# Performance work log

Hardware: AMD Instinct MI355X
Metric: run time of the kernel (lower is better)

Reference implementation:

```python
import jax, jax.numpy as jnp
import numpy as np

HEIGHT = 8
WIDTH = 8
C = 3
FEAT = HEIGHT * WIDTH * C  # 192
ENC = 16


def setup_inputs() -> dict:
    key = jax.random.key(0)
    k1, k2, k3, k4, k5 = jax.random.split(key, 5)
    B, H, W = 128, 256, 256
    x = jax.random.normal(k1, (B, C, H, W), dtype=jnp.float32)
    # torch Linear init ~ U(-1/sqrt(fan_in), 1/sqrt(fan_in))
    s1 = 1.0 / np.sqrt(FEAT)
    s2 = 1.0 / np.sqrt(ENC)
    W_enc = jax.random.uniform(k2, (ENC, FEAT), jnp.float32, -s1, s1)
    b_enc = jax.random.uniform(k3, (ENC,), jnp.float32, -s1, s1)
    W_dec = jax.random.uniform(k4, (FEAT, ENC), jnp.float32, -s2, s2)
    b_dec = jax.random.uniform(k5, (FEAT,), jnp.float32, -s2, s2)
    return {"x": x, "W_enc": W_enc, "b_enc": b_enc, "W_dec": W_dec, "b_dec": b_dec}


def reference(x, W_enc, b_enc, W_dec, b_dec):
    B, Cc, H, W = x.shape
    nh, nw = H // HEIGHT, W // WIDTH
    # Extract non-overlapping patches, flattened in (C, h, w) order to match
    # x[:, :, i:i+h, j:j+w].reshape(B, -1) in the original.
    xp = x.reshape(B, Cc, nh, HEIGHT, nw, WIDTH)
    xp = xp.transpose(0, 2, 4, 1, 3, 5).reshape(B, nh, nw, FEAT)  # [B,nh,nw,FEAT]
    h = jax.nn.relu(jnp.einsum('bijf,ef->bije', xp, W_enc) + b_enc)
    out = jax.nn.relu(jnp.einsum('bije,fe->bijf', h, W_dec) + b_dec)
    attention = jax.nn.softmax(out, axis=-1)
    out = attention * out
    # Scatter patches back into image layout.
    y = out.reshape(B, nh, nw, Cc, HEIGHT, WIDTH).transpose(0, 3, 1, 4, 2, 5)
    y = y.reshape(B, Cc, H, W)
    return y
```

## Files before the change

kernel.cpp:

```cpp
#include <hip/hip_runtime.h>


constexpr int NPATCH = 128 * 32 * 32;
constexpr float L2E  = 1.4426950408889634f;

__device__ __forceinline__ float rdlane(float v, int l) {
  return __uint_as_float(__builtin_amdgcn_readlane(__float_as_uint(v), l));
}

__global__ __launch_bounds__(512, 4) void spatial_attn(
    const float* __restrict__ x,
    const float* __restrict__ Wenc,
    const float* __restrict__ benc,
    const float* __restrict__ Wdec,
    const float* __restrict__ bdec,
    float* __restrict__ y)
{
  __shared__ float  encl[16 * 512];
  __shared__ float2 hl2[8 * 64];
  __shared__ float  sls[512];

  const int tid  = threadIdx.x;
  const int lane = tid & 63;
  const int wv   = __builtin_amdgcn_readfirstlane(tid >> 6);
  const int p    = blockIdx.x * 64 + lane;
  const int b    = p >> 10;
  const int ii   = (p >> 5) & 31;
  const int jj   = p & 31;
  const size_t base = (size_t)b * 196608 + (size_t)ii * 2048 + (size_t)jj * 8;

  float we[16];
  const int col = (lane < 24) ? lane : 0;
  #pragma unroll
  for (int e = 0; e < 16; ++e) we[e] = Wenc[e * 192 + wv * 24 + col];

  float2 xv2[12];
  #pragma unroll
  for (int t = 0; t < 3; ++t) {
    const int cr = 3 * wv + t;
    const float* src = x + base + (cr >> 3) * 65536 + (cr & 7) * 256;
    const float4 v0 = *(const float4*)(src);
    const float4 v1 = *(const float4*)(src + 4);
    xv2[t*4+0] = make_float2(v0.x, v0.y);
    xv2[t*4+1] = make_float2(v0.z, v0.w);
    xv2[t*4+2] = make_float2(v1.x, v1.y);
    xv2[t*4+3] = make_float2(v1.z, v1.w);
  }

  #pragma unroll
  for (int e = 0; e < 16; ++e) {
    float2 a2 = make_float2(0.0f, 0.0f);
    #pragma unroll
    for (int k = 0; k < 12; ++k) {
      a2.x = fmaf(rdlane(we[e], 2 * k),     xv2[k].x, a2.x);
      a2.y = fmaf(rdlane(we[e], 2 * k + 1), xv2[k].y, a2.y);
    }
    encl[e * 512 + tid] = a2.x + a2.y;
  }
  __syncthreads();

  {
    const int e0 = 2 * wv;
    const float* c0 = encl + e0 * 512 + lane;
    const float* c1 = c0 + 512;
    float a0 = c0[0], a1 = c1[0];
    #pragma unroll
    for (int w8 = 1; w8 < 8; ++w8) { a0 += c0[w8 * 64]; a1 += c1[w8 * 64]; }
    hl2[wv * 64 + lane] = make_float2(fmaxf(a0 + benc[e0],     0.0f),
                                      fmaxf(a1 + benc[e0 + 1], 0.0f));
  }
  __syncthreads();

  float2 h2[8];
  #pragma unroll
  for (int k = 0; k < 8; ++k) h2[k] = hl2[k * 64 + lane];

  float o[24];
  float s = 0.0f;
  #pragma unroll
  for (int q = 0; q < 24; ++q) {
    const int f = wv * 24 + q;
    const float2* w2 = (const float2*)(Wdec + f * 16);
    float2 a2 = make_float2(bdec[f], 0.0f);
    #pragma unroll
    for (int k = 0; k < 8; ++k) {
      a2.x = fmaf(w2[k].x, h2[k].x, a2.x);
      a2.y = fmaf(w2[k].y, h2[k].y, a2.y);
    }
    float v = fmaxf(a2.x + a2.y, 0.0f);
    o[q] = v;
    s += __builtin_amdgcn_exp2f(v * L2E);
  }

  sls[tid] = s;
  __syncthreads();
  float st = sls[lane];
  #pragma unroll
  for (int w8 = 1; w8 < 8; ++w8) st += sls[w8 * 64 + lane];
  const float inv = __builtin_amdgcn_rcpf(st);

  #pragma unroll
  for (int t = 0; t < 3; ++t) {
    const int cr = 3 * wv + t;
    float* dst = y + base + (cr >> 3) * 65536 + (cr & 7) * 256;
    float r[8];
    #pragma unroll
    for (int c = 0; c < 8; ++c) {
      const float ov = o[t * 8 + c];
      r[c] = __builtin_amdgcn_exp2f(ov * L2E) * inv * ov;
    }
    const float4 s0 = {r[0], r[1], r[2], r[3]};
    const float4 s1 = {r[4], r[5], r[6], r[7]};
    *(float4*)(dst)     = s0;
    *(float4*)(dst + 4) = s1;
  }
}

extern "C" void kernel_launch(void* const* d_in, const int* in_sizes, int n_in,
                              void* d_out, int out_size, void* d_ws, size_t ws_size,
                              hipStream_t stream) {
  const float* x    = (const float*)d_in[0];
  const float* Wenc = (const float*)d_in[1];
  const float* benc = (const float*)d_in[2];
  const float* Wdec = (const float*)d_in[3];
  const float* bdec = (const float*)d_in[4];
  float* y = (float*)d_out;
  dim3 grid(NPATCH / 64), block(512);
  hipLaunchKernelGGL(spatial_attn, grid, block, 0, stream, x, Wenc, benc, Wdec, bdec, y);
}
```

Measured before the change: 193.8 us.

## Process two patch groups per block with prefetch of second input tile

Each 512-thread block now handles 128 patches in two phases instead of 64, and the grid is halved. The input for the second group is loaded while the first group's encoder results are being reduced and decoded, to hide global memory latency. Encoder weights are now read as wave-uniform scalar loads rather than lane broadcasts. Decoder weights are held in registers and broadcast with readlane. The aim is to overlap loads with compute and amortise weight loads, at the cost of more registers and fewer blocks.

```diff
diff --git a/kernel.cpp b/kernel.cpp
--- a/kernel.cpp
+++ b/kernel.cpp
@@ -23,43 +23,48 @@
   const int tid  = threadIdx.x;
   const int lane = tid & 63;
   const int wv   = __builtin_amdgcn_readfirstlane(tid >> 6);
-  const int p    = blockIdx.x * 64 + lane;
-  const int b    = p >> 10;
-  const int ii   = (p >> 5) & 31;
-  const int jj   = p & 31;
-  const size_t base = (size_t)b * 196608 + (size_t)ii * 2048 + (size_t)jj * 8;
+  const int p0   = blockIdx.x * 128 + lane;
+  const int b    = p0 >> 10;
+  const int ii   = (p0 >> 5) & 31;
+  const int jj   = p0 & 31;
+  const size_t base0 = (size_t)b * 196608 + (size_t)ii * 2048 + (size_t)jj * 8;
+  const size_t base1 = base0 + 4096;
 
-  float we[16];
-  const int col = (lane < 24) ? lane : 0;
+  float wd[6];
   #pragma unroll
-  for (int e = 0; e < 16; ++e) we[e] = Wenc[e * 192 + wv * 24 + col];
+  for (int k = 0; k < 6; ++k) wd[k] = Wdec[wv * 384 + k * 64 + lane];
 
   float2 xv2[12];
-  #pragma unroll
-  for (int t = 0; t < 3; ++t) {
-    const int cr = 3 * wv + t;
-    const float* src = x + base + (cr >> 3) * 65536 + (cr & 7) * 256;
-    const float4 v0 = *(const float4*)(src);
-    const float4 v1 = *(const float4*)(src + 4);
-    xv2[t*4+0] = make_float2(v0.x, v0.y);
-    xv2[t*4+1] = make_float2(v0.z, v0.w);
-    xv2[t*4+2] = make_float2(v1.x, v1.y);
-    xv2[t*4+3] = make_float2(v1.z, v1.w);
-  }
 
-  #pragma unroll
-  for (int e = 0; e < 16; ++e) {
-    float2 a2 = make_float2(0.0f, 0.0f);
+  auto loadx = [&](size_t base) {
     #pragma unroll
-    for (int k = 0; k < 12; ++k) {
-      a2.x = fmaf(rdlane(we[e], 2 * k),     xv2[k].x, a2.x);
-      a2.y = fmaf(rdlane(we[e], 2 * k + 1), xv2[k].y, a2.y);
+    for (int t = 0; t < 3; ++t) {
+      const int cr = 3 * wv + t;
+      const float* src = x + base + (cr >> 3) * 65536 + (cr & 7) * 256;
+      const float4 v0 = *(const float4*)(src);
+      const float4 v1 = *(const float4*)(src + 4);
+      xv2[t*4+0] = make_float2(v0.x, v0.y);
+      xv2[t*4+1] = make_float2(v0.z, v0.w);
+      xv2[t*4+2] = make_float2(v1.x, v1.y);
+      xv2[t*4+3] = make_float2(v1.z, v1.w);
     }
-    encl[e * 512 + tid] = a2.x + a2.y;
-  }
-  __syncthreads();
+  };
 
-  {
+  auto encode = [&]() {
+    #pragma unroll
+    for (int e = 0; e < 16; ++e) {
+      const float* w = Wenc + e * 192 + wv * 24;
+      float2 a2 = make_float2(0.0f, 0.0f);
+      #pragma unroll
+      for (int k = 0; k < 12; ++k) {
+        a2.x = fmaf(w[2*k],   xv2[k].x, a2.x);
+        a2.y = fmaf(w[2*k+1], xv2[k].y, a2.y);
+      }
+      encl[e * 512 + tid] = a2.x + a2.y;
+    }
+  };
+
+  auto reduce = [&]() {
     const int e0 = 2 * wv;
     const float* c0 = encl + e0 * 512 + lane;
     const float* c1 = c0 + 512;
@@ -68,52 +73,76 @@
     for (int w8 = 1; w8 < 8; ++w8) { a0 += c0[w8 * 64]; a1 += c1[w8 * 64]; }
     hl2[wv * 64 + lane] = make_float2(fmaxf(a0 + benc[e0],     0.0f),
                                       fmaxf(a1 + benc[e0 + 1], 0.0f));
-  }
+  };
+
+  float o[24];
+
+  auto decode = [&](const float2* h2, float& s) {
+    s = 0.0f;
+    #pragma unroll
+    for (int q = 0; q < 24; ++q) {
+      const int f = wv * 24 + q;
+      float v = bdec[f];
+      #pragma unroll
+      for (int e = 0; e < 16; ++e) {
+        const int idx = q * 16 + e;
+        v = fmaf(rdlane(wd[idx >> 6], idx & 63), h2[e >> 1].x * (1 - (e & 1)) +
+                 h2[e >> 1].y * (e & 1), v);
+      }
+      v = fmaxf(v, 0.0f);
+      o[q] = v;
+      s += __builtin_amdgcn_exp2f(v * L2E);
+    }
+  };
+
+  auto epilogue = [&](size_t base, float inv) {
+    #pragma unroll
+    for (int t = 0; t < 3; ++t) {
+      const int cr = 3 * wv + t;
+      float* dst = y + base + (cr >> 3) * 65536 + (cr & 7) * 256;
+      float r[8];
+      #pragma unroll
+      for (int c = 0; c < 8; ++c) {
+        const float ov = o[t * 8 + c];
+        r[c] = __builtin_amdgcn_exp2f(ov * L2E) * inv * ov;
+      }
+      *(float4*)(dst)     = (float4){r[0], r[1], r[2], r[3]};
+      *(float4*)(dst + 4) = (float4){r[4], r[5], r[6], r[7]};
+    }
+  };
+
+  loadx(base0);
+  encode();
+  loadx(base1);
   __syncthreads();
-
+  reduce();
+  __syncthreads();
   float2 h2[8];
   #pragma unroll
   for (int k = 0; k < 8; ++k) h2[k] = hl2[k * 64 + lane];
-
-  float o[24];
-  float s = 0.0f;
-  #pragma unroll
-  for (int q = 0; q < 24; ++q) {
-    const int f = wv * 24 + q;
-    const float2* w2 = (const float2*)(Wdec + f * 16);
-    float2 a2 = make_float2(bdec[f], 0.0f);
-    #pragma unroll
-    for (int k = 0; k < 8; ++k) {
-      a2.x = fmaf(w2[k].x, h2[k].x, a2.x);
-      a2.y = fmaf(w2[k].y, h2[k].y, a2.y);
-    }
-    float v = fmaxf(a2.x + a2.y, 0.0f);
-    o[q] = v;
-    s += __builtin_amdgcn_exp2f(v * L2E);
-  }
-
-  sls[tid] = s;
+  float sA;
+  decode(h2, sA);
+  sls[tid] = sA;
   __syncthreads();
   float st = sls[lane];
   #pragma unroll
   for (int w8 = 1; w8 < 8; ++w8) st += sls[w8 * 64 + lane];
-  const float inv = __builtin_amdgcn_rcpf(st);
+  epilogue(base0, __builtin_amdgcn_rcpf(st));
 
+  encode();
+  __syncthreads();
+  reduce();
+  __syncthreads();
   #pragma unroll
-  for (int t = 0; t < 3; ++t) {
-    const int cr = 3 * wv + t;
-    float* dst = y + base + (cr >> 3) * 65536 + (cr & 7) * 256;
-    float r[8];
-    #pragma unroll
-    for (int c = 0; c < 8; ++c) {
-      const float ov = o[t * 8 + c];
-      r[c] = __builtin_amdgcn_exp2f(ov * L2E) * inv * ov;
-    }
-    const float4 s0 = {r[0], r[1], r[2], r[3]};
-    const float4 s1 = {r[4], r[5], r[6], r[7]};
-    *(float4*)(dst)     = s0;
-    *(float4*)(dst + 4) = s1;
-  }
+  for (int k = 0; k < 8; ++k) h2[k] = hl2[k * 64 + lane];
+  float sB;
+  decode(h2, sB);
+  sls[tid] = sB;
+  __syncthreads();
+  st = sls[lane];
+  #pragma unroll
+  for (int w8 = 1; w8 < 8; ++w8) st += sls[w8 * 64 + lane];
+  epilogue(base1, __builtin_amdgcn_rcpf(st));
 }
 
 extern "C" void kernel_launch(void* const* d_in, const int* in_sizes, int n_in,
@@ -125,6 +154,6 @@
   const float* Wdec = (const float*)d_in[3];
   const float* bdec = (const float*)d_in[4];
   float* y = (float*)d_out;
-  dim3 grid(NPATCH / 64), block(512);
+  dim3 grid(NPATCH / 128), block(512);
   hipLaunchKernelGGL(spatial_attn, grid, block, 0, stream, x, Wenc, benc, Wdec, bdec, y);
 }
```

Result: slower. 208.1 us (+7.4%).
